# Kernel tuning notes

Hardware: AMD Instinct MI355X
Metric: run time of the kernel (lower is better)

## Reference

```python
import jax, jax.numpy as jnp
import numpy as np

NUM_QUBIT = 20
NUM_LAYERS = 4
DIM = 2 ** NUM_QUBIT

# constant CNOT (control kind gate: apply X on target when control=1)
_CNOT = jnp.array([[1, 0, 0, 0],
                   [0, 1, 0, 0],
                   [0, 0, 0, 1],
                   [0, 0, 1, 0]], dtype=jnp.complex64)


def _ry(t):
    # hf0 for a parameterized single-qubit rotation gate Ry(theta)
    c = jnp.cos(t / 2)
    s = jnp.sin(t / 2)
    return jnp.stack([jnp.stack([c, -s]), jnp.stack([s, c])]).astype(jnp.complex64)


def _apply_1q(state, u2, q):
    # state: (2,)*n complex; contract gate on qubit axis q (numqi.sim.state.apply_gate)
    out = jnp.tensordot(u2, state, axes=((1,), (q,)))
    return jnp.moveaxis(out, 0, q)


def _apply_2q(state, u4, q0, q1):
    # 4x4 two-qubit gate on axes (q0, q1) (covers apply_control_n_gate for CNOT)
    out = jnp.tensordot(u4.reshape(2, 2, 2, 2), state, axes=((2, 3), (q0, q1)))
    return jnp.moveaxis(out, (0, 1), (q0, q1))


def setup_inputs() -> dict:
    key = jax.random.key(0)
    k1, k2, k3 = jax.random.split(key, 3)
    theta = jax.random.normal(k1, (NUM_LAYERS, NUM_QUBIT), dtype=jnp.float32)
    qr = jax.random.normal(k2, (DIM,), dtype=jnp.float32)
    qi = jax.random.normal(k3, (DIM,), dtype=jnp.float32)
    # normalize initial state vector
    nrm = jnp.sqrt(jnp.sum(qr * qr + qi * qi))
    return {"theta": theta, "q0_real": qr / nrm, "q0_imag": qi / nrm}


def reference(theta, q0_real, q0_imag):
    # forward of _CircuitFunction: sequential gate application on the state vector
    state = (q0_real.astype(jnp.complex64) + 1j * q0_imag.astype(jnp.complex64))
    state = state.reshape((2,) * NUM_QUBIT)
    for layer in range(NUM_LAYERS):
        for q in range(NUM_QUBIT):          # parameterized 'unitary' gates
            state = _apply_1q(state, _ry(theta[layer, q]), q)
        for q in range(NUM_QUBIT - 1):      # constant 'control' gates (CNOT chain)
            state = _apply_2q(state, _CNOT, q, q + 1)
    flat = state.reshape(DIM)
    # return real/imag stacked so output dtype is real float32
    return jnp.stack([jnp.real(flat), jnp.imag(flat)])
```

## Files before the change

### kernel.cpp

```cpp
#include <hip/hip_runtime.h>
#include <cstdint>

#define NQ 20
#define DIM (1u << NQ)

typedef float f32x2 __attribute__((ext_vector_type(2)));
typedef float f32x4 __attribute__((ext_vector_type(4)));

constexpr unsigned cpair_mask(int l, int b) {
    unsigned m = 1u << b;
    for (int k = 0; k < l; ++k) m ^= m >> 1;
    return m;
}
constexpr unsigned cginv1(unsigned x) {
    x ^= x >> 1; x ^= x >> 2; x ^= x >> 4; x ^= x >> 8; x ^= x >> 16;
    return x & 0xFFFFFu;
}
constexpr unsigned csel_mask(int l, int b) {
    unsigned R = 0;
    for (int k = 0; k < NQ; ++k) {
        unsigned w = 1u << k;
        for (int t = 0; t < l; ++t) w = cginv1(w);
        if ((w >> b) & 1u) R |= 1u << k;
    }
    return R;
}
constexpr unsigned cswz(unsigned t) { return t ^ ((t >> 5) & 0xFu); }

struct GateC { unsigned R; unsigned sb; int valid; int tix; int thix; };
struct GroupC { int pv[2]; unsigned gxs[4]; unsigned lgxs[4]; GateC gt[2]; };
struct SchedC { GroupC g[20]; int bar[20]; int ng; };
struct PhC { SchedC s; int FL, GAP; };

constexpr unsigned to_local(unsigned m, int FL, int GAP) {
    return (m & ((1u << FL) - 1u)) | ((m >> (FL + GAP)) << FL);
}

constexpr void addg(SchedC& s, int FL, int GAP, int bar,
                    int l0, int b0, int l1, int b1) {
    GroupC g{};
    int ls[2] = {l0, l1}; int bs[2] = {b0, b1};
    unsigned m[2] = {0, 0};
    for (int j = 0; j < 2; ++j) {
        bool val = ls[j] >= 0;
        m[j] = val ? cpair_mask(ls[j], bs[j]) : (1u << bs[j]);
        g.gt[j].R = val ? csel_mask(ls[j], bs[j]) : 0u;
        g.gt[j].valid = val ? 1 : 0;
        g.gt[j].tix = val ? (ls[j] * NQ + bs[j]) : 0;
        g.gt[j].thix = val ? (ls[j] * NQ + (NQ - 1 - bs[j])) : 0;
    }
    for (int e = 0; e < 4; ++e) {
        unsigned x = ((e & 1) ? m[0] : 0u) ^ ((e & 2) ? m[1] : 0u);
        g.gxs[e] = x;
        g.lgxs[e] = to_local(x, FL, GAP);
    }
    for (int j = 0; j < 2; ++j) {
        unsigned sb = 0;
        for (int e = 0; e < 4; ++e)
            if (__builtin_popcount(g.gxs[e] & g.gt[j].R) & 1) sb |= (1u << e);
        g.gt[j].sb = sb;
    }
    int pv[2] = {0, 0};
    for (int j = 0; j < 2; ++j) {
        unsigned lm = to_local(m[j], FL, GAP);
        int p = 0; for (int k = 0; k < 12; ++k) if ((lm >> k) & 1) p = k;
        pv[j] = p;
    }
    if (pv[0] > pv[1]) { int t = pv[0]; pv[0] = pv[1]; pv[1] = t; }
    g.pv[0] = pv[0]; g.pv[1] = pv[1];
    s.bar[s.ng] = bar;
    s.g[s.ng] = g; s.ng++;
}

constexpr PhC mk_phase(int ph) {
    PhC P{};
    if (ph == 0) {
        P.FL = 12; P.GAP = 8;
        addg(P.s, 12, 8, 0, 0,0, 0,1);
        addg(P.s, 12, 8, 1, 0,2, 0,3);
        addg(P.s, 12, 8, 0, 0,4, 0,5);
        addg(P.s, 12, 8, 0, 0,6, 0,7);
        addg(P.s, 12, 8, 1, 0,8, 0,9);
        addg(P.s, 12, 8, 1, 0,10, 0,11);
    } else if (ph == 1) {
        P.FL = 4; P.GAP = 8;
        addg(P.s, 4, 8, 0, 0,12, 0,13);
        addg(P.s, 4, 8, 1, 0,14, 0,15);
        addg(P.s, 4, 8, 1, 0,16, 0,17);
        addg(P.s, 4, 8, 1, 0,18, 0,19);
        addg(P.s, 4, 8, 1, 1,13, 1,14);
        addg(P.s, 4, 8, 1, 1,15, 1,16);
        addg(P.s, 4, 8, 1, 1,17, 1,18);
        addg(P.s, 4, 8, 1, 1,19, 2,14);
        addg(P.s, 4, 8, 1, 2,15, 2,16);
        addg(P.s, 4, 8, 1, 2,17, 2,18);
        addg(P.s, 4, 8, 1, 2,19, 3,15);
        addg(P.s, 4, 8, 1, 3,16, 3,17);
        addg(P.s, 4, 8, 1, 3,18, 3,19);
    } else if (ph == 2) {
        P.FL = 6; P.GAP = 3;
        addg(P.s, 6, 3, 0, 1,10, 1,11);
        addg(P.s, 6, 3, 1, 1,12, 2,11);
        addg(P.s, 6, 3, 1, 2,12, 2,13);
        addg(P.s, 6, 3, 1, 3,12, 3,13);
        addg(P.s, 6, 3, 1, 3,14, -1,0);
    } else {
        P.FL = 12; P.GAP = 8;
        addg(P.s, 12, 8, 0, 1,0, 1,1);
        addg(P.s, 12, 8, 1, 1,2, 1,3);
        addg(P.s, 12, 8, 0, 1,4, 1,5);
        addg(P.s, 12, 8, 0, 1,6, 1,7);
        addg(P.s, 12, 8, 1, 1,8, 1,9);
        addg(P.s, 12, 8, 1, 2,0, 2,1);
        addg(P.s, 12, 8, 0, 2,2, 2,3);
        addg(P.s, 12, 8, 0, 2,4, 2,5);
        addg(P.s, 12, 8, 0, 2,6, 2,7);
        addg(P.s, 12, 8, 1, 2,8, 2,9);
        addg(P.s, 12, 8, 1, 2,10, 3,2);
        addg(P.s, 12, 8, 1, 3,3, 3,4);
        addg(P.s, 12, 8, 0, 3,5, 3,6);
        addg(P.s, 12, 8, 1, 3,7, 3,8);
        addg(P.s, 12, 8, 1, 3,9, 3,10);
        addg(P.s, 12, 8, 1, 3,11, -1,0);
        addg(P.s, 12, 8, 1, 3,0, 3,1);
    }
    return P;
}

constexpr bool pivots_ok(int ph) {
    PhC P = mk_phase(ph);
    for (int i = 0; i < P.s.ng; ++i)
        if (P.s.g[i].pv[0] == P.s.g[i].pv[1]) return false;
    return true;
}
constexpr bool window_ok(int ph) {
    PhC P = mk_phase(ph);
    for (int i = 0; i < P.s.ng; ++i)
        for (int e = 0; e < 4; ++e) {
            unsigned lm = P.s.g[i].lgxs[e];
            unsigned inv = (lm & ((1u << P.FL) - 1u)) | ((lm >> P.FL) << (P.FL + P.GAP));
            if (inv != P.s.g[i].gxs[e]) return false;
        }
    return true;
}
constexpr bool order_ok() {
    int el[96] = {}, eb[96] = {}; int n = 0;
    for (int ph = 0; ph < 4; ++ph) {
        PhC P = mk_phase(ph);
        for (int gi = 0; gi < P.s.ng; ++gi)
            for (int j = 0; j < 2; ++j)
                if (P.s.g[gi].gt[j].valid) {
                    el[n] = P.s.g[gi].gt[j].tix / NQ;
                    eb[n] = P.s.g[gi].gt[j].tix % NQ;
                    ++n;
                }
    }
    if (n != 80) return false;
    bool seen[80] = {};
    unsigned M[80] = {}, R[80] = {};
    for (int i = 0; i < n; ++i) {
        int idx = el[i] * NQ + eb[i];
        if (seen[idx]) return false;
        seen[idx] = true;
        M[i] = cpair_mask(el[i], eb[i]);
        R[i] = csel_mask(el[i], eb[i]);
    }
    for (int i = 0; i < n; ++i)
        for (int j = i + 1; j < n; ++j)
            if (el[i] > el[j]) {
                int p1 = __builtin_popcount(M[i] & R[j]) & 1;
                int p2 = __builtin_popcount(M[j] & R[i]) & 1;
                if (p1 != p2) return false;
            }
    return true;
}
static_assert(pivots_ok(0) && pivots_ok(1) && pivots_ok(2) && pivots_ok(3),
              "pivot collision: coset decomposition not bijective");
static_assert(window_ok(0) && window_ok(1) && window_ok(2) && window_ok(3),
              "gate mask outside phase window");
static_assert(order_ok(), "executed gate order not circuit-equivalent");

constexpr unsigned max_gxs(const GroupC& g) {
    unsigned m = 0;
    for (int e = 0; e < 4; ++e) if (g.gxs[e] > m) m = g.gxs[e];
    return m;
}

__device__ __forceinline__ unsigned swz(unsigned t) { return t ^ ((t >> 5) & 0xFu); }
__device__ __forceinline__ f32x2 splat2(float x) { f32x2 r = {x, x}; return r; }

template<int FL, int GAP>
__device__ __forceinline__ unsigned gmapF(unsigned t, unsigned mid) {
    if constexpr (FL == 12) return (mid << 12) | t;
    else return (t & ((1u << FL) - 1u)) | ((mid & ((1u << GAP) - 1u)) << FL)
              | ((t >> FL) << (FL + GAP)) | ((mid >> GAP) << (GAP + 12));
}

__device__ __forceinline__ unsigned expand2(unsigned u, int p0, int p1) {
    u = ((u >> p0) << (p0 + 1)) | (u & ((1u << p0) - 1u));
    u = ((u >> p1) << (p1 + 1)) | (u & ((1u << p1) - 1u));
    return u;
}

#define APPLY_GROUP(G, v, g0, cd, sd)                                           \
    {                                                                            \
        _Pragma("unroll")                                                        \
        for (int j = 0; j < 2; ++j) {                                            \
            if ((G).gt[j].valid) {                                               \
                const f32x2 cc_ = splat2((cd)[j]);                               \
                const unsigned par_ = (unsigned)__popc((g0) & (G).gt[j].R) & 1u; \
                const float sp_ = par_ ? (sd)[j] : -(sd)[j];                     \
                _Pragma("unroll")                                                \
                for (int pr = 0; pr < 2; ++pr) {                                 \
                    const int ea = (j == 0) ? (pr << 1) : pr;                    \
                    const int eb = ea | (1 << j);                                \
                    const f32x2 sg_ = splat2((((G).gt[j].sb >> ea) & 1u) ? -sp_ : sp_); \
                    const f32x2 a_ = v[ea], b_ = v[eb];                          \
                    v[ea] = cc_ * a_ + sg_ * b_;                                 \
                    v[eb] = cc_ * b_ - sg_ * a_;                                 \
                }                                                                \
            }                                                                    \
        }                                                                        \
    }

template<int PH, bool IS_INIT, bool IS_FINAL>
__global__ __launch_bounds__(1024) void k_phase(f32x2* __restrict__ st,
                                                const float* __restrict__ qr,
                                                const float* __restrict__ qi,
                                                const float* __restrict__ theta,
                                                float* __restrict__ out) {
    constexpr PhC P = mk_phase(PH);
    constexpr int FL = P.FL, GAP = P.GAP, NG = P.s.ng;
    __shared__ __align__(16) f32x2 lds[4096];
    __shared__ float2 trigS[80];
    const unsigned tid = threadIdx.x;
    const unsigned mid = blockIdx.x;

    if (tid < 80) {
        int l = tid / NQ, b = tid % NQ;
        float th = 0.5f * theta[l * NQ + (NQ - 1 - b)];
        trigS[tid] = make_float2(cosf(th), sinf(th));
    }

    {
        constexpr GroupC G = P.s.g[0];
        constexpr bool CIN = (max_gxs(G) < 4u);
        const unsigned t0 = expand2(tid, G.pv[0], G.pv[1]);
        const unsigned g0 = gmapF<FL, GAP>(t0, mid);
        f32x2 v[4];
        if constexpr (IS_INIT) {
            const f32x4* r4 = reinterpret_cast<const f32x4*>(qr);
            const f32x4* i4 = reinterpret_cast<const f32x4*>(qi);
            f32x4 ra = r4[g0 >> 2], ia = i4[g0 >> 2];
            const float re[4] = {ra.x, ra.y, ra.z, ra.w};
            const float im[4] = {ia.x, ia.y, ia.z, ia.w};
#pragma unroll
            for (int e = 0; e < 4; ++e) v[e] = f32x2{re[G.gxs[e] & 3u], im[G.gxs[e] & 3u]};
        } else if constexpr (CIN) {
            const f32x4* s4 = reinterpret_cast<const f32x4*>(st);
            f32x4 q[2];
            q[0] = s4[g0 >> 1]; q[1] = s4[(g0 >> 1) + 1];
            const float* qq = reinterpret_cast<const float*>(q);
#pragma unroll
            for (int e = 0; e < 4; ++e) {
                const unsigned j = G.gxs[e] & 3u;
                v[e] = f32x2{qq[2 * j], qq[2 * j + 1]};
            }
        } else {
#pragma unroll
            for (int e = 0; e < 4; ++e) v[e] = st[g0 ^ G.gxs[e]];
        }
        float cd[2], sd[2];
#pragma unroll
        for (int j = 0; j < 2; ++j)
            if (G.gt[j].valid) {
                float th = 0.5f * theta[G.gt[j].thix];
                cd[j] = cosf(th); sd[j] = sinf(th);
            }
        APPLY_GROUP(G, v, g0, cd, sd);
#pragma unroll
        for (int e = 0; e < 4; ++e) lds[swz(t0 ^ G.lgxs[e])] = v[e];
    }

#pragma unroll
    for (int gi = 1; gi < NG - 1; ++gi) {
        if (P.s.bar[gi]) __syncthreads();
        else __builtin_amdgcn_wave_barrier();
        const unsigned t0 = expand2(tid, P.s.g[gi].pv[0], P.s.g[gi].pv[1]);
        const unsigned g0 = gmapF<FL, GAP>(t0, mid);
        const unsigned sz0 = swz(t0);
        f32x2 v[4]; unsigned ad[4];
#pragma unroll
        for (int e = 0; e < 4; ++e) {
            ad[e] = sz0 ^ cswz(P.s.g[gi].lgxs[e]);
            v[e] = lds[ad[e]];
        }
        float cd[2], sd[2];
#pragma unroll
        for (int j = 0; j < 2; ++j)
            if (P.s.g[gi].gt[j].valid) {
                float2 cs = trigS[P.s.g[gi].gt[j].tix];
                cd[j] = cs.x; sd[j] = cs.y;
            }
        APPLY_GROUP(P.s.g[gi], v, g0, cd, sd);
#pragma unroll
        for (int e = 0; e < 4; ++e) lds[ad[e]] = v[e];
    }

    __syncthreads();

    {
        constexpr GroupC G = P.s.g[NG - 1];
        const unsigned t0 = expand2(tid, G.pv[0], G.pv[1]);
        const unsigned g0 = gmapF<FL, GAP>(t0, mid);
        f32x2 v[4];
#pragma unroll
        for (int e = 0; e < 4; ++e) v[e] = lds[swz(t0 ^ G.lgxs[e])];
        float cd[2], sd[2];
#pragma unroll
        for (int j = 0; j < 2; ++j)
            if (G.gt[j].valid) {
                float2 cs = trigS[G.gt[j].tix];
                cd[j] = cs.x; sd[j] = cs.y;
            }
        APPLY_GROUP(G, v, g0, cd, sd);
        if constexpr (IS_FINAL) {
            const unsigned i0 = g0 ^ (g0 >> 4) ^ (g0 >> 8) ^ (g0 >> 12) ^ (g0 >> 16);
            const unsigned base = i0 & ~3u;
            const unsigned lo = i0 & 3u;
            f32x2 u[4];
#pragma unroll
            for (int e = 0; e < 4; ++e) u[G.gxs[e] & 3u] = v[e];
#pragma unroll
            for (int bit = 1; bit <= 2; bit <<= 1) {
                const bool c = (lo & (unsigned)bit) != 0u;
                f32x2 t[4];
#pragma unroll
                for (int k = 0; k < 4; ++k) t[k] = c ? u[k ^ bit] : u[k];
#pragma unroll
                for (int k = 0; k < 4; ++k) u[k] = t[k];
            }
            float4* oR = reinterpret_cast<float4*>(out + base);
            float4* oI = reinterpret_cast<float4*>(out + DIM + base);
            oR[0] = make_float4(u[0].x, u[1].x, u[2].x, u[3].x);
            oI[0] = make_float4(u[0].y, u[1].y, u[2].y, u[3].y);
        } else {
#pragma unroll
            for (int e = 0; e < 4; ++e) st[g0 ^ G.gxs[e]] = v[e];
        }
    }
}

extern "C" void kernel_launch(void* const* d_in, const int* in_sizes, int n_in,
                              void* d_out, int out_size, void* d_ws, size_t ws_size,
                              hipStream_t stream) {
    const float* theta = (const float*)d_in[0];
    const float* qr    = (const float*)d_in[1];
    const float* qi    = (const float*)d_in[2];
    float* out = (float*)d_out;
    f32x2* st = (f32x2*)d_ws;

    k_phase<0, true,  false><<<256, 1024, 0, stream>>>(st, qr, qi, theta, out);
    k_phase<1, false, false><<<256, 1024, 0, stream>>>(st, qr, qi, theta, out);
    k_phase<2, false, false><<<256, 1024, 0, stream>>>(st, qr, qi, theta, out);
    k_phase<3, false, true ><<<256, 1024, 0, stream>>>(st, qr, qi, theta, out);
}
```

Baseline: 43.10 us.

## Fuse a third gate into groups whose pair mask equals m0 xor m1

Extends gate groups to hold up to three rotation gates, where the third gate's pair mask is the XOR of the first two. The four loaded amplitudes can then take an extra gate with no additional LDS round trip. Phases 1, 2 and 3 are rescheduled into fewer groups, which removes some LDS passes and barriers. This relies on the compile-time checks holding for gate reordering, and it adds register and arithmetic work per group.

```diff
diff --git a/kernel.cpp b/kernel.cpp
--- a/kernel.cpp
+++ b/kernel.cpp
@@ -28,7 +28,7 @@
 constexpr unsigned cswz(unsigned t) { return t ^ ((t >> 5) & 0xFu); }
 
 struct GateC { unsigned R; unsigned sb; int valid; int tix; int thix; };
-struct GroupC { int pv[2]; unsigned gxs[4]; unsigned lgxs[4]; GateC gt[2]; };
+struct GroupC { int pv[2]; unsigned gxs[4]; unsigned lgxs[4]; GateC gt[3]; unsigned m01[2]; };
 struct SchedC { GroupC g[20]; int bar[20]; int ng; };
 struct PhC { SchedC s; int FL, GAP; };
 
@@ -37,24 +37,25 @@
 }
 
 constexpr void addg(SchedC& s, int FL, int GAP, int bar,
-                    int l0, int b0, int l1, int b1) {
+                    int l0, int b0, int l1, int b1, int l2, int b2) {
     GroupC g{};
-    int ls[2] = {l0, l1}; int bs[2] = {b0, b1};
+    int ls[3] = {l0, l1, l2}; int bs[3] = {b0, b1, b2};
     unsigned m[2] = {0, 0};
-    for (int j = 0; j < 2; ++j) {
+    for (int j = 0; j < 3; ++j) {
         bool val = ls[j] >= 0;
-        m[j] = val ? cpair_mask(ls[j], bs[j]) : (1u << bs[j]);
+        if (j < 2) m[j] = val ? cpair_mask(ls[j], bs[j]) : (1u << bs[j]);
         g.gt[j].R = val ? csel_mask(ls[j], bs[j]) : 0u;
         g.gt[j].valid = val ? 1 : 0;
         g.gt[j].tix = val ? (ls[j] * NQ + bs[j]) : 0;
         g.gt[j].thix = val ? (ls[j] * NQ + (NQ - 1 - bs[j])) : 0;
     }
+    g.m01[0] = m[0]; g.m01[1] = m[1];
     for (int e = 0; e < 4; ++e) {
         unsigned x = ((e & 1) ? m[0] : 0u) ^ ((e & 2) ? m[1] : 0u);
         g.gxs[e] = x;
         g.lgxs[e] = to_local(x, FL, GAP);
     }
-    for (int j = 0; j < 2; ++j) {
+    for (int j = 0; j < 3; ++j) {
         unsigned sb = 0;
         for (int e = 0; e < 4; ++e)
             if (__builtin_popcount(g.gxs[e] & g.gt[j].R) & 1) sb |= (1u << e);
@@ -76,53 +77,50 @@
     PhC P{};
     if (ph == 0) {
         P.FL = 12; P.GAP = 8;
-        addg(P.s, 12, 8, 0, 0,0, 0,1);
-        addg(P.s, 12, 8, 1, 0,2, 0,3);
-        addg(P.s, 12, 8, 0, 0,4, 0,5);
-        addg(P.s, 12, 8, 0, 0,6, 0,7);
-        addg(P.s, 12, 8, 1, 0,8, 0,9);
-        addg(P.s, 12, 8, 1, 0,10, 0,11);
+        addg(P.s, 12, 8, 0, 0,0, 0,1, -1,0);
+        addg(P.s, 12, 8, 1, 0,2, 0,3, -1,0);
+        addg(P.s, 12, 8, 0, 0,4, 0,5, -1,0);
+        addg(P.s, 12, 8, 0, 0,6, 0,7, -1,0);
+        addg(P.s, 12, 8, 1, 0,8, 0,9, -1,0);
+        addg(P.s, 12, 8, 1, 0,10, 0,11, -1,0);
     } else if (ph == 1) {
         P.FL = 4; P.GAP = 8;
-        addg(P.s, 4, 8, 0, 0,12, 0,13);
-        addg(P.s, 4, 8, 1, 0,14, 0,15);
-        addg(P.s, 4, 8, 1, 0,16, 0,17);
-        addg(P.s, 4, 8, 1, 0,18, 0,19);
-        addg(P.s, 4, 8, 1, 1,13, 1,14);
-        addg(P.s, 4, 8, 1, 1,15, 1,16);
-        addg(P.s, 4, 8, 1, 1,17, 1,18);
-        addg(P.s, 4, 8, 1, 1,19, 2,14);
-        addg(P.s, 4, 8, 1, 2,15, 2,16);
-        addg(P.s, 4, 8, 1, 2,17, 2,18);
-        addg(P.s, 4, 8, 1, 2,19, 3,15);
-        addg(P.s, 4, 8, 1, 3,16, 3,17);
-        addg(P.s, 4, 8, 1, 3,18, 3,19);
+        addg(P.s, 4, 8, 0, 0,12, 0,13, -1,0);
+        addg(P.s, 4, 8, 1, 0,14, 0,15, -1,0);
+        addg(P.s, 4, 8, 1, 0,16, 0,17, -1,0);
+        addg(P.s, 4, 8, 1, 0,18, 0,19, 1,19);
+        addg(P.s, 4, 8, 1, 1,13, 1,14, -1,0);
+        addg(P.s, 4, 8, 1, 1,15, 1,16, -1,0);
+        addg(P.s, 4, 8, 1, 1,17, 1,18, 2,18);
+        addg(P.s, 4, 8, 1, 2,14, 2,15, -1,0);
+        addg(P.s, 4, 8, 1, 2,19, -1,0, -1,0);
+        addg(P.s, 4, 8, 1, 2,16, 2,17, 3,17);
+        addg(P.s, 4, 8, 1, 3,15, 3,16, -1,0);
+        addg(P.s, 4, 8, 1, 3,18, 3,19, -1,0);
     } else if (ph == 2) {
         P.FL = 6; P.GAP = 3;
-        addg(P.s, 6, 3, 0, 1,10, 1,11);
-        addg(P.s, 6, 3, 1, 1,12, 2,11);
-        addg(P.s, 6, 3, 1, 2,12, 2,13);
-        addg(P.s, 6, 3, 1, 3,12, 3,13);
-        addg(P.s, 6, 3, 1, 3,14, -1,0);
+        addg(P.s, 6, 3, 0, 1,11, 1,12, 2,12);
+        addg(P.s, 6, 3, 1, 1,10, 2,11, -1,0);
+        addg(P.s, 6, 3, 1, 2,13, 3,12, -1,0);
+        addg(P.s, 6, 3, 1, 3,13, 3,14, -1,0);
     } else {
         P.FL = 12; P.GAP = 8;
-        addg(P.s, 12, 8, 0, 1,0, 1,1);
-        addg(P.s, 12, 8, 1, 1,2, 1,3);
-        addg(P.s, 12, 8, 0, 1,4, 1,5);
-        addg(P.s, 12, 8, 0, 1,6, 1,7);
-        addg(P.s, 12, 8, 1, 1,8, 1,9);
-        addg(P.s, 12, 8, 1, 2,0, 2,1);
-        addg(P.s, 12, 8, 0, 2,2, 2,3);
-        addg(P.s, 12, 8, 0, 2,4, 2,5);
-        addg(P.s, 12, 8, 0, 2,6, 2,7);
-        addg(P.s, 12, 8, 1, 2,8, 2,9);
-        addg(P.s, 12, 8, 1, 2,10, 3,2);
-        addg(P.s, 12, 8, 1, 3,3, 3,4);
-        addg(P.s, 12, 8, 0, 3,5, 3,6);
-        addg(P.s, 12, 8, 1, 3,7, 3,8);
-        addg(P.s, 12, 8, 1, 3,9, 3,10);
-        addg(P.s, 12, 8, 1, 3,11, -1,0);
-        addg(P.s, 12, 8, 1, 3,0, 3,1);
+        addg(P.s, 12, 8, 0, 1,0, 1,1, -1,0);
+        addg(P.s, 12, 8, 1, 1,2, 1,3, -1,0);
+        addg(P.s, 12, 8, 0, 1,4, 1,5, -1,0);
+        addg(P.s, 12, 8, 0, 1,6, 1,7, -1,0);
+        addg(P.s, 12, 8, 1, 1,8, 1,9, 2,9);
+        addg(P.s, 12, 8, 1, 2,0, 2,1, -1,0);
+        addg(P.s, 12, 8, 0, 2,2, 2,3, -1,0);
+        addg(P.s, 12, 8, 0, 2,4, 2,5, -1,0);
+        addg(P.s, 12, 8, 0, 2,6, 2,7, -1,0);
+        addg(P.s, 12, 8, 1, 2,8, 2,10, -1,0);
+        addg(P.s, 12, 8, 1, 3,2, 3,3, -1,0);
+        addg(P.s, 12, 8, 0, 3,4, 3,5, -1,0);
+        addg(P.s, 12, 8, 0, 3,6, 3,7, -1,0);
+        addg(P.s, 12, 8, 1, 3,8, 3,9, -1,0);
+        addg(P.s, 12, 8, 1, 3,10, 3,11, -1,0);
+        addg(P.s, 12, 8, 1, 3,0, 3,1, -1,0);
     }
     return P;
 }
@@ -143,12 +141,21 @@
         }
     return true;
 }
+constexpr bool triples_ok(int ph) {
+    PhC P = mk_phase(ph);
+    for (int i = 0; i < P.s.ng; ++i)
+        if (P.s.g[i].gt[2].valid) {
+            int l = P.s.g[i].gt[2].tix / NQ, b = P.s.g[i].gt[2].tix % NQ;
+            if (cpair_mask(l, b) != (P.s.g[i].m01[0] ^ P.s.g[i].m01[1])) return false;
+        }
+    return true;
+}
 constexpr bool order_ok() {
     int el[96] = {}, eb[96] = {}; int n = 0;
     for (int ph = 0; ph < 4; ++ph) {
         PhC P = mk_phase(ph);
         for (int gi = 0; gi < P.s.ng; ++gi)
-            for (int j = 0; j < 2; ++j)
+            for (int j = 0; j < 3; ++j)
                 if (P.s.g[gi].gt[j].valid) {
                     el[n] = P.s.g[gi].gt[j].tix / NQ;
                     eb[n] = P.s.g[gi].gt[j].tix % NQ;
@@ -178,6 +185,8 @@
               "pivot collision: coset decomposition not bijective");
 static_assert(window_ok(0) && window_ok(1) && window_ok(2) && window_ok(3),
               "gate mask outside phase window");
+static_assert(triples_ok(0) && triples_ok(1) && triples_ok(2) && triples_ok(3),
+              "third gate mask != m0^m1");
 static_assert(order_ok(), "executed gate order not circuit-equivalent");
 
 constexpr unsigned max_gxs(const GroupC& g) {
@@ -205,15 +214,16 @@
 #define APPLY_GROUP(G, v, g0, cd, sd)                                           \
     {                                                                            \
         _Pragma("unroll")                                                        \
-        for (int j = 0; j < 2; ++j) {                                            \
+        for (int j = 0; j < 3; ++j) {                                            \
             if ((G).gt[j].valid) {                                               \
                 const f32x2 cc_ = splat2((cd)[j]);                               \
                 const unsigned par_ = (unsigned)__popc((g0) & (G).gt[j].R) & 1u; \
                 const float sp_ = par_ ? (sd)[j] : -(sd)[j];                     \
+                const int xr_ = (j == 0) ? 1 : ((j == 1) ? 2 : 3);               \
                 _Pragma("unroll")                                                \
                 for (int pr = 0; pr < 2; ++pr) {                                 \
                     const int ea = (j == 0) ? (pr << 1) : pr;                    \
-                    const int eb = ea | (1 << j);                                \
+                    const int eb = ea ^ xr_;                                     \
                     const f32x2 sg_ = splat2((((G).gt[j].sb >> ea) & 1u) ? -sp_ : sp_); \
                     const f32x2 a_ = v[ea], b_ = v[eb];                          \
                     v[ea] = cc_ * a_ + sg_ * b_;                                 \
@@ -270,9 +280,9 @@
 #pragma unroll
             for (int e = 0; e < 4; ++e) v[e] = st[g0 ^ G.gxs[e]];
         }
-        float cd[2], sd[2];
-#pragma unroll
-        for (int j = 0; j < 2; ++j)
+        float cd[3], sd[3];
+#pragma unroll
+        for (int j = 0; j < 3; ++j)
             if (G.gt[j].valid) {
                 float th = 0.5f * theta[G.gt[j].thix];
                 cd[j] = cosf(th); sd[j] = sinf(th);
@@ -295,9 +305,9 @@
             ad[e] = sz0 ^ cswz(P.s.g[gi].lgxs[e]);
             v[e] = lds[ad[e]];
         }
-        float cd[2], sd[2];
-#pragma unroll
-        for (int j = 0; j < 2; ++j)
+        float cd[3], sd[3];
+#pragma unroll
+        for (int j = 0; j < 3; ++j)
             if (P.s.g[gi].gt[j].valid) {
                 float2 cs = trigS[P.s.g[gi].gt[j].tix];
                 cd[j] = cs.x; sd[j] = cs.y;
@@ -316,9 +326,9 @@
         f32x2 v[4];
 #pragma unroll
         for (int e = 0; e < 4; ++e) v[e] = lds[swz(t0 ^ G.lgxs[e])];
-        float cd[2], sd[2];
-#pragma unroll
-        for (int j = 0; j < 2; ++j)
+        float cd[3], sd[3];
+#pragma unroll
+        for (int j = 0; j < 3; ++j)
             if (G.gt[j].valid) {
                 float2 cs = trigS[G.gt[j].tix];
                 cd[j] = cs.x; sd[j] = cs.y;
```

New measurement: 42.16 us (median of 2 runs). -2.2%, faster.
